# Optimization experiments

Hardware: AMD Instinct MI355X
Metric: run time of the kernel (lower is better)

## Reference

```python
import math
import jax, jax.numpy as jnp
import numpy as np

N_FLOWS = 5
DIM = 64
NH = 128          # hidden multiplier -> hidden width = DIM*NH = 8192
BATCH = 4096


def _masks(out_f, in_f, dim):
    od, idd = out_f // dim, in_f // dim
    mask_d = np.zeros((out_f, in_f), np.float32)
    mask_o = np.ones((out_f, in_f), np.float32)
    for i in range(dim):
        mask_d[i * od:(i + 1) * od, i * idd:(i + 1) * idd] = 1.0
        mask_o[i * od:(i + 1) * od, i * idd:] = 0.0
    return jnp.asarray(mask_d), jnp.asarray(mask_o)

MASK_D1, MASK_O1 = _masks(DIM * NH, DIM, DIM)   # layer 1: (H, D)
MASK_D2, MASK_O2 = _masks(DIM, DIM * NH, DIM)   # layer 2: (D, H)


def masked_weight(x, W, dw, b, mask_d, mask_o, dim, grad=None):
    """MaskedWeight.forward. W:(out,in), dw:(out,1), b:(out,)."""
    out_f, in_f = W.shape
    od, idd = out_f // dim, in_f // dim
    w = jnp.exp(W) * mask_d + W * mask_o                 # (out, in)
    wsn = jnp.sum(w * w, axis=-1, keepdims=True)         # (out, 1)
    wn = jnp.exp(dw) * w / jnp.sqrt(wsn)                 # weight-normalized
    wpl = dw + W - 0.5 * jnp.log(wsn)                    # (out, in)
    # extract diagonal blocks of wpl^T: (dim, idd, od)
    blocks = wpl.reshape(dim, od, dim, idd)
    wpl_t = blocks[np.arange(dim), :, np.arange(dim), :].transpose(0, 2, 1)
    y = x @ wn.T + b                                     # (B, out)
    g = wpl_t.transpose(0, 2, 1)                         # (dim, od, idd)
    if grad is None:
        new_grad = jnp.broadcast_to(g[None], (x.shape[0],) + g.shape)
    else:
        # logsumexp over contracted block axis: out (B, dim, od, b_prev)
        new_grad = jax.nn.logsumexp(
            g[None, :, :, None, :] + jnp.swapaxes(grad, -2, -1)[:, :, None, :, :],
            axis=-1)
    return y, new_grad


def tanh_layer(x, grad):
    g = -2.0 * (x - math.log(2.0) + jax.nn.softplus(-2.0 * x))
    return jnp.tanh(x), g.reshape(grad.shape) + grad


def bnaf_flow(x, W1, d1, b1, W2, d2, b2, gate):
    h, g = masked_weight(x, W1, d1, b1, MASK_D1, MASK_O1, DIM)
    h, g = tanh_layer(h, g)
    y, g = masked_weight(h, W2, d2, b2, MASK_D2, MASK_O2, DIM, grad=g)
    grad = g[:, :, 0, 0]                                  # (B, DIM) -- squeeze
    if gate is None:                                      # res=None (last flow)
        return y, jnp.sum(grad, axis=-1)
    s = jax.nn.sigmoid(gate)                              # res='gated'
    out = s * y + (1.0 - s) * x
    ld = jnp.sum(jax.nn.softplus(grad + gate) - jax.nn.softplus(gate), axis=-1)
    return out, ld


def setup_inputs() -> dict:
    key = jax.random.key(0)
    ks = jax.random.split(key, 8)
    H = DIM * NH
    return {
        "x":  jax.random.normal(ks[0], (BATCH, DIM), jnp.float32),
        "W1": jax.random.normal(ks[1], (N_FLOWS, H, DIM), jnp.float32) * 0.1,
        "d1": jax.random.normal(ks[2], (N_FLOWS, H, 1), jnp.float32) * 0.1,
        "b1": jax.random.normal(ks[3], (N_FLOWS, H), jnp.float32) * 0.01,
        "W2": jax.random.normal(ks[4], (N_FLOWS, DIM, H), jnp.float32) * 0.1,
        "d2": jax.random.normal(ks[5], (N_FLOWS, DIM, 1), jnp.float32) * 0.1,
        "b2": jax.random.normal(ks[6], (N_FLOWS, DIM), jnp.float32) * 0.01,
        "gates": jax.random.normal(ks[7], (N_FLOWS - 1,), jnp.float32),
    }


def reference(x, W1, d1, b1, W2, d2, b2, gates):
    log_det = jnp.zeros(x.shape[0], x.dtype)
    for f in range(N_FLOWS):
        gate = gates[f] if f < N_FLOWS - 1 else None
        x, ld = bnaf_flow(x, W1[f], d1[f], b1[f], W2[f], d2[f], b2[f], gate)
        log_det = log_det + ld
        if f < N_FLOWS - 1:                               # Permutation 'flip'
            x = x[:, ::-1]
    return x, log_det
```

## Files before the change

kernel.cpp:

```cpp
#include <hip/hip_runtime.h>
#include <hip/hip_bf16.h>
#include <math.h>

#define NFLOWS 5
#define DIMF 64
#define HID 8192
#define BATCHN 4096

typedef unsigned int u32;
typedef __bf16 bf16x8 __attribute__((ext_vector_type(8)));
typedef float f32x4 __attribute__((ext_vector_type(4)));

__device__ __forceinline__ short f2bf_s(float x){
  u32 b = __float_as_uint(x);
  b += 0x7fff + ((b >> 16) & 1);
  return (short)(b >> 16);
}
__device__ __forceinline__ u32 pk_bf16(float a, float b){
#if __has_builtin(__builtin_amdgcn_cvt_pk_bf16_f32)
  typedef __bf16 bf16x2_t __attribute__((ext_vector_type(2)));
  bf16x2_t r = __builtin_amdgcn_cvt_pk_bf16_f32(a, b);
  return __builtin_bit_cast(u32, r);
#else
  u32 x = __float_as_uint(a); x += 0x7fff + ((x >> 16) & 1);
  u32 y = __float_as_uint(b); y += 0x7fff + ((y >> 16) & 1);
  return (x >> 16) | (y & 0xffff0000u);
#endif
}
__device__ __forceinline__ float softplus_f(float z){
  return fmaxf(z, 0.f) + log1pf(__expf(-fabsf(z)));
}

__global__ __launch_bounds__(256) void prep_fused_kernel(
    const float* __restrict__ W1, const float* __restrict__ d1,
    const float* __restrict__ b1,
    const float* __restrict__ W2, const float* __restrict__ d2,
    short* __restrict__ wn1s, short* __restrict__ wn2s,
    float* __restrict__ bec, float* __restrict__ cmax)
{
  __shared__ float g1s[128];
  __shared__ float cbuf[128];
  __shared__ float red[4];
  __shared__ float Msh;

  const int tid  = threadIdx.x;
  const int w    = tid >> 6;
  const int lane = tid & 63;
  const int f    = blockIdx.x >> 6;
  const int i    = blockIdx.x & 63;

  {
    const int ks2 = lane >> 5, q = (lane & 31) >> 3, j = lane & 7;
    #pragma unroll 4
    for (int it = 0; it < 32; ++it) {
      int rr = w * 32 + it;
      size_t R = (size_t)(f * HID + i * 128 + rr);
      float Wv = W1[R * 64 + lane];
      float wv = (lane == i) ? __expf(Wv) : ((lane < i) ? Wv : 0.f);
      float sq = wv * wv;
      #pragma unroll
      for (int m = 1; m < 64; m <<= 1) sq += __shfl_xor(sq, m, 64);
      float d1v = d1[R];
      float sc = __expf(d1v) * rsqrtf(sq);
      int nt = rr >> 4, n16 = rr & 15;
      size_t dst = ((((size_t)(f * 64 + i) * 8 + nt) * 2 + ks2) << 9)
                 + ((q * 16 + n16) << 3) + j;
      wn1s[dst] = f2bf_s(wv * sc);
      if (lane == i) g1s[rr] = d1v + Wv - 0.5f * __logf(sq);
    }
  }
  __syncthreads();

  const float* Wrow = W2 + ((size_t)(f * DIMF + i)) * HID;
  const float d2v = d2[f * DIMF + i];

  float part = 0.f;
  #pragma unroll
  for (int it = 0; it < 4; ++it) {
    int k0 = it * 2048 + tid * 8;
    int kb = k0 >> 7;
    float4 a = *(const float4*)(Wrow + k0);
    float4 b = *(const float4*)(Wrow + k0 + 4);
    float wv[8] = {a.x, a.y, a.z, a.w, b.x, b.y, b.z, b.w};
    if (kb == i) {
      #pragma unroll
      for (int e = 0; e < 8; ++e) wv[e] = __expf(wv[e]);
    } else if (kb > i) {
      #pragma unroll
      for (int e = 0; e < 8; ++e) wv[e] = 0.f;
    }
    #pragma unroll
    for (int e = 0; e < 8; ++e) part = fmaf(wv[e], wv[e], part);
  }
  #pragma unroll
  for (int m = 1; m < 64; m <<= 1) part += __shfl_xor(part, m, 64);
  if (lane == 0) red[w] = part;
  __syncthreads();
  float wsn = red[0] + red[1] + red[2] + red[3];
  float ls = __logf(wsn);
  float sc = __expf(d2v) * rsqrtf(wsn);

  const int mt2 = i >> 4, c16r = i & 15;
  #pragma unroll
  for (int it = 0; it < 4; ++it) {
    int k0 = it * 2048 + tid * 8;
    int kb = k0 >> 7;
    float4 a = *(const float4*)(Wrow + k0);
    float4 b = *(const float4*)(Wrow + k0 + 4);
    float wv[8] = {a.x, a.y, a.z, a.w, b.x, b.y, b.z, b.w};
    if (kb == i) {
      int rr0 = k0 - i * 128;
      #pragma unroll
      for (int e = 0; e < 8; ++e) {
        cbuf[rr0 + e] = g1s[rr0 + e] + d2v + wv[e] - 0.5f * ls;
        wv[e] = __expf(wv[e]);
      }
    } else if (kb > i) {
      #pragma unroll
      for (int e = 0; e < 8; ++e) wv[e] = 0.f;
    }
    int ib = k0 >> 7, ks = (k0 >> 5) & 3, qq = (k0 >> 3) & 3;
    size_t dst = ((((size_t)(f * 64 + ib) * 4 + ks) * 4 + mt2) << 9)
               + ((qq * 16 + c16r) << 3);
    uint4 pk4;
    pk4.x = pk_bf16(wv[0]*sc, wv[1]*sc); pk4.y = pk_bf16(wv[2]*sc, wv[3]*sc);
    pk4.z = pk_bf16(wv[4]*sc, wv[5]*sc); pk4.w = pk_bf16(wv[6]*sc, wv[7]*sc);
    *(uint4*)(wn2s + dst) = pk4;
  }
  __syncthreads();

  if (w == 0) {
    float m = fmaxf(cbuf[lane], cbuf[lane + 64]);
    #pragma unroll
    for (int s = 1; s < 64; s <<= 1) m = fmaxf(m, __shfl_xor(m, s, 64));
    if (lane == 0) { cmax[f * DIMF + i] = m; Msh = m; }
  }
  __syncthreads();
  float M = Msh;

  if (tid < 128) {
    int k = i * 128 + tid;
    float2 v;
    v.x = b1[f * HID + k];
    v.y = 4.f * __expf(cbuf[tid] - M);
    *(float2*)(bec + (((size_t)(f * HID + k)) << 1)) = v;
  }
}

__global__ __launch_bounds__(1024, 4)
void bnaf_main_kernel(
    const float* __restrict__ x_in,
    const float* __restrict__ b2,
    const float* __restrict__ gates,
    const short* __restrict__ wn1s,
    const short* __restrict__ wn2s,
    const float* __restrict__ bec, const float* __restrict__ cmax,
    float* __restrict__ out)
{
  __shared__ __attribute__((aligned(16))) char smem[146816];
  float* xs  = (float*)smem;
  short* xbS = (short*)(smem + 4352);
  float* ldp = (float*)(smem + 145792);

  const int tid  = threadIdx.x;
  const int w    = tid >> 6;
  const int lane = tid & 63;
  const int c16  = lane & 15;
  const int q    = lane >> 4;
  const int r0   = blockIdx.x * 16;

  short* tbuf0 = (short*)(smem + 6528 + w * 8704);
  short* tbuf1 = (short*)(smem + 6528 + w * 8704 + 4352);

  {
    int row = tid >> 6, col = tid & 63;
    float v = x_in[((size_t)(r0 + row) << 6) | col];
    xs[row * 68 + col] = v;
    xbS[(col >> 3) * 136 + row * 8 + (col & 7)] = f2bf_s(v);
  }
  float ldtot = 0.f;
  __syncthreads();

  #pragma unroll 1
  for (int f = 0; f < NFLOWS; ++f) {
    const float gatev = (f < NFLOWS - 1) ? gates[f] : 0.f;
    const float spg   = (f < NFLOWS - 1) ? softplus_f(gatev) : 0.f;

    f32x4 yacc[4];
    #pragma unroll
    for (int n = 0; n < 4; ++n) yacc[n] = f32x4{0.f, 0.f, 0.f, 0.f};
    float ldacc = 0.f;

    #pragma unroll 1
    for (int ii = 0; ii < 4; ++ii) {
      const int i = ii * 16 + w;
      short* tb = (ii & 1) ? tbuf1 : tbuf0;
      const short* p1l = wn1s + (((size_t)(f * 64 + i)) << 13) + lane * 8;
      const float* becp = bec + (((size_t)(f * HID + i * 128 + q * 4)) << 1);
      const bool hiHalf = (i >= 32);

      float s0 = 0.f, s1 = 0.f;
      f32x4 dd[4];

      {
        const bf16x8 xa0 = *(const bf16x8*)(xbS + q * 136 + c16 * 8);
        #pragma unroll
        for (int nt = 0; nt < 4; ++nt) {
          f32x4 z = {0.f, 0.f, 0.f, 0.f};
          bf16x8 bw0 = *(const bf16x8*)(p1l + nt * 1024);
          dd[nt] = __builtin_amdgcn_mfma_f32_16x16x32_bf16(bw0, xa0, z, 0, 0, 0);
        }
        if (hiHalf) {
          const bf16x8 xa1 = *(const bf16x8*)(xbS + (4 + q) * 136 + c16 * 8);
          #pragma unroll
          for (int nt = 0; nt < 4; ++nt) {
            bf16x8 bw1 = *(const bf16x8*)(p1l + nt * 1024 + 512);
            dd[nt] = __builtin_amdgcn_mfma_f32_16x16x32_bf16(bw1, xa1, dd[nt], 0, 0, 0);
          }
        }
      }
      #pragma unroll
      for (int nt = 0; nt < 4; ++nt) {
        float4 e0 = *(const float4*)(becp + nt * 32);
        float4 e1 = *(const float4*)(becp + nt * 32 + 4);
        float t[4];
        #pragma unroll
        for (int r = 0; r < 4; ++r) {
          float bb = (r == 0) ? e0.x : (r == 1) ? e0.z : (r == 2) ? e1.x : e1.z;
          float ee = (r == 0) ? e0.y : (r == 1) ? e0.w : (r == 2) ? e1.y : e1.w;
          float h  = dd[nt][r] + bb;
          float up = __expf(-2.f * fabsf(h));
          float vp = __builtin_amdgcn_rcpf(1.f + up);
          float ta = fmaf(-2.f * up, vp, 1.f);
          t[r] = copysignf(ta, h);
          float c1 = ee * up, c2 = vp * vp;
          if (r & 1) s1 = fmaf(c1, c2, s1); else s0 = fmaf(c1, c2, s0);
        }
        uint2 pk; pk.x = pk_bf16(t[0], t[1]); pk.y = pk_bf16(t[2], t[3]);
        *(uint2*)(tb + c16 * 136 + nt * 16 + q * 4) = pk;
      }

      if (ii > 0) {
        const int ip = i - 16;
        short* tp = ((ii - 1) & 1) ? tbuf1 : tbuf0;
        asm volatile("s_waitcnt lgkmcnt(0)" ::: "memory");
        const short* p2l = wn2s + (((size_t)(f * 64 + ip)) << 13) + lane * 8;
        const int mt0 = ip >> 4;
        #pragma unroll
        for (int ks = 0; ks < 4; ++ks) {
          bf16x8 tfrag = *(const bf16x8*)(tp + c16 * 136 + ks * 32 + q * 8);
          #pragma unroll
          for (int mt = 0; mt < 4; ++mt) {
            if (mt >= mt0) {
              bf16x8 wb = *(const bf16x8*)(p2l + (ks * 4 + mt) * 512);
              yacc[mt] = __builtin_amdgcn_mfma_f32_16x16x32_bf16(wb, tfrag, yacc[mt], 0, 0, 0);
            }
          }
        }
      }

      {
        const bf16x8 xa0 = *(const bf16x8*)(xbS + q * 136 + c16 * 8);
        #pragma unroll
        for (int nt = 0; nt < 4; ++nt) {
          f32x4 z = {0.f, 0.f, 0.f, 0.f};
          bf16x8 bw0 = *(const bf16x8*)(p1l + (nt + 4) * 1024);
          dd[nt] = __builtin_amdgcn_mfma_f32_16x16x32_bf16(bw0, xa0, z, 0, 0, 0);
        }
        if (hiHalf) {
          const bf16x8 xa1 = *(const bf16x8*)(xbS + (4 + q) * 136 + c16 * 8);
          #pragma unroll
          for (int nt = 0; nt < 4; ++nt) {
            bf16x8 bw1 = *(const bf16x8*)(p1l + (nt + 4) * 1024 + 512);
            dd[nt] = __builtin_amdgcn_mfma_f32_16x16x32_bf16(bw1, xa1, dd[nt], 0, 0, 0);
          }
        }
      }
      #pragma unroll
      for (int nt = 0; nt < 4; ++nt) {
        float4 e0 = *(const float4*)(becp + (nt + 4) * 32);
        float4 e1 = *(const float4*)(becp + (nt + 4) * 32 + 4);
        float t[4];
        #pragma unroll
        for (int r = 0; r < 4; ++r) {
          float bb = (r == 0) ? e0.x : (r == 1) ? e0.z : (r == 2) ? e1.x : e1.z;
          float ee = (r == 0) ? e0.y : (r == 1) ? e0.w : (r == 2) ? e1.y : e1.w;
          float h  = dd[nt][r] + bb;
          float up = __expf(-2.f * fabsf(h));
          float vp = __builtin_amdgcn_rcpf(1.f + up);
          float ta = fmaf(-2.f * up, vp, 1.f);
          t[r] = copysignf(ta, h);
          float c1 = ee * up, c2 = vp * vp;
          if (r & 1) s1 = fmaf(c1, c2, s1); else s0 = fmaf(c1, c2, s0);
        }
        uint2 pk; pk.x = pk_bf16(t[0], t[1]); pk.y = pk_bf16(t[2], t[3]);
        *(uint2*)(tb + c16 * 136 + (nt + 4) * 16 + q * 4) = pk;
      }

      float sacc = s0 + s1;
      sacc += __shfl_xor(sacc, 16, 64);
      sacc += __shfl_xor(sacc, 32, 64);
      const float Mi = cmax[f * DIMF + i];
      float grad = Mi + __logf(sacc);
      ldacc += (f < NFLOWS - 1) ? (softplus_f(grad + gatev) - spg) : grad;
    }

    {
      const int ip = 48 + w;
      asm volatile("s_waitcnt lgkmcnt(0)" ::: "memory");
      const short* p2l = wn2s + (((size_t)(f * 64 + ip)) << 13) + lane * 8;
      const int mt0 = ip >> 4;
      #pragma unroll
      for (int ks = 0; ks < 4; ++ks) {
        bf16x8 tfrag = *(const bf16x8*)(tbuf1 + c16 * 136 + ks * 32 + q * 8);
        #pragma unroll
        for (int mt = 0; mt < 4; ++mt) {
          if (mt >= mt0) {
            bf16x8 wb = *(const bf16x8*)(p2l + (ks * 4 + mt) * 512);
            yacc[mt] = __builtin_amdgcn_mfma_f32_16x16x32_bf16(wb, tfrag, yacc[mt], 0, 0, 0);
          }
        }
      }
    }

    float* ypw = (float*)(smem + 6528 + w * 8704);
    #pragma unroll
    for (int mt = 0; mt < 4; ++mt)
      #pragma unroll
      for (int r = 0; r < 4; ++r)
        ypw[(mt * 4 + r) * 65 + lane] = yacc[mt][r];
    if (q == 0) ldp[w * 16 + c16] = ldacc;
    __syncthreads();

    float sgate = 0.f;
    if (f < NFLOWS - 1) sgate = __builtin_amdgcn_rcpf(1.f + __expf(-gatev));
    int row = tid >> 6, col = tid & 63;
    int idx = ((col >> 4) * 4 + (col & 3)) * 65 + (((col >> 2) & 3) * 16 + row);
    float v = b2[f * DIMF + col];
    #pragma unroll
    for (int ww = 0; ww < 16; ++ww)
      v += ((const float*)(smem + 6528 + ww * 8704))[idx];
    float nx = 0.f; int nrow = 0, ncol = 0;
    if (f < NFLOWS - 1) {
      float xv = xs[row * 68 + col];
      nx = fmaf(sgate, v - xv, xv);
      nrow = row; ncol = 63 - col;
    } else {
      out[((size_t)(r0 + row) << 6) | col] = v;
    }
    if (tid < 16) {
      float a = 0.f;
      #pragma unroll
      for (int ww = 0; ww < 16; ++ww) a += ldp[ww * 16 + tid];
      ldtot += a;
    }
    __syncthreads();
    if (f < NFLOWS - 1) {
      xs[nrow * 68 + ncol] = nx;
      xbS[(ncol >> 3) * 136 + nrow * 8 + (ncol & 7)] = f2bf_s(nx);
      __syncthreads();
    }
  }

  if (tid < 16) out[(size_t)BATCHN * DIMF + r0 + tid] = ldtot;
}

extern "C" void kernel_launch(void* const* d_in, const int* in_sizes, int n_in,
                              void* d_out, int out_size, void* d_ws, size_t ws_size,
                              hipStream_t stream)
{
  const float* x     = (const float*)d_in[0];
  const float* W1    = (const float*)d_in[1];
  const float* d1    = (const float*)d_in[2];
  const float* b1    = (const float*)d_in[3];
  const float* W2    = (const float*)d_in[4];
  const float* d2    = (const float*)d_in[5];
  const float* b2    = (const float*)d_in[6];
  const float* gates = (const float*)d_in[7];
  float* out = (float*)d_out;

  char* ws = (char*)d_ws;
  short* wn1s  = (short*)ws;
  short* wn2s  = (short*)(ws + 5242880);
  float* bec   = (float*)(ws + 10485760);
  float* cmaxp = (float*)(ws + 10813440);

  hipLaunchKernelGGL(prep_fused_kernel, dim3(320), dim3(256), 0, stream,
                     W1, d1, b1, W2, d2, wn1s, wn2s, bec, cmaxp);
  hipLaunchKernelGGL(bnaf_main_kernel, dim3(256), dim3(1024), 0, stream,
                     x, b2, gates, wn1s, wn2s, bec, cmaxp, out);
}
```

Measured before the change: 322.3 us.

## Halve main-kernel block rows, widen prep kernel, fold bias into MFMA accumulator

The main kernel now processes 8 batch rows per block with 8 waves (512 blocks), padding the MFMA input to 16 rows with zeros and halving LDS use so more blocks can be resident. Each wave now loops over 8 hidden blocks instead of 4, and the waves hand off in steps of 8. The layer-1 bias is loaded directly as the MFMA accumulator initialiser, and the interleaved bias/exp buffer is replaced by a plain exp-constant array. The prep kernel uses 1024 threads so each thread reads its W2 slice once instead of twice. The trade-off is that half of each MFMA's rows are wasted padding, and every block re-reads the full weight set, doubling total weight traffic.

```diff
diff --git a/kernel.cpp b/kernel.cpp
--- a/kernel.cpp
+++ b/kernel.cpp
@@ -31,16 +31,15 @@
   return fmaxf(z, 0.f) + log1pf(__expf(-fabsf(z)));
 }
 
-__global__ __launch_bounds__(256) void prep_fused_kernel(
+__global__ __launch_bounds__(1024) void prep_fused_kernel(
     const float* __restrict__ W1, const float* __restrict__ d1,
-    const float* __restrict__ b1,
     const float* __restrict__ W2, const float* __restrict__ d2,
     short* __restrict__ wn1s, short* __restrict__ wn2s,
-    float* __restrict__ bec, float* __restrict__ cmax)
+    float* __restrict__ expc4, float* __restrict__ cmax)
 {
   __shared__ float g1s[128];
   __shared__ float cbuf[128];
-  __shared__ float red[4];
+  __shared__ float red[16];
   __shared__ float Msh;
 
   const int tid  = threadIdx.x;
@@ -51,9 +50,9 @@
 
   {
     const int ks2 = lane >> 5, q = (lane & 31) >> 3, j = lane & 7;
-    #pragma unroll 4
-    for (int it = 0; it < 32; ++it) {
-      int rr = w * 32 + it;
+    #pragma unroll
+    for (int it = 0; it < 8; ++it) {
+      int rr = w * 8 + it;
       size_t R = (size_t)(f * HID + i * 128 + rr);
       float Wv = W1[R * 64 + lane];
       float wv = (lane == i) ? __expf(Wv) : ((lane < i) ? Wv : 0.f);
@@ -73,58 +72,46 @@
 
   const float* Wrow = W2 + ((size_t)(f * DIMF + i)) * HID;
   const float d2v = d2[f * DIMF + i];
-
+  const int k0 = tid * 8;
+  const int kb = tid >> 4;
+  float4 a = *(const float4*)(Wrow + k0);
+  float4 b = *(const float4*)(Wrow + k0 + 4);
+  float wv[8] = {a.x, a.y, a.z, a.w, b.x, b.y, b.z, b.w};
+  const bool diag = (kb == i);
+  float cv[8];
+  float mv[8];
+  #pragma unroll
+  for (int e = 0; e < 8; ++e) {
+    if (diag)        { cv[e] = g1s[(k0 - i * 128) + e] + d2v + wv[e]; mv[e] = __expf(wv[e]); }
+    else if (kb > i) { mv[e] = 0.f; }
+    else             { mv[e] = wv[e]; }
+  }
   float part = 0.f;
   #pragma unroll
-  for (int it = 0; it < 4; ++it) {
-    int k0 = it * 2048 + tid * 8;
-    int kb = k0 >> 7;
-    float4 a = *(const float4*)(Wrow + k0);
-    float4 b = *(const float4*)(Wrow + k0 + 4);
-    float wv[8] = {a.x, a.y, a.z, a.w, b.x, b.y, b.z, b.w};
-    if (kb == i) {
-      #pragma unroll
-      for (int e = 0; e < 8; ++e) wv[e] = __expf(wv[e]);
-    } else if (kb > i) {
-      #pragma unroll
-      for (int e = 0; e < 8; ++e) wv[e] = 0.f;
-    }
-    #pragma unroll
-    for (int e = 0; e < 8; ++e) part = fmaf(wv[e], wv[e], part);
-  }
+  for (int e = 0; e < 8; ++e) part = fmaf(mv[e], mv[e], part);
   #pragma unroll
   for (int m = 1; m < 64; m <<= 1) part += __shfl_xor(part, m, 64);
   if (lane == 0) red[w] = part;
   __syncthreads();
-  float wsn = red[0] + red[1] + red[2] + red[3];
+  float wsn = 0.f;
+  #pragma unroll
+  for (int e = 0; e < 16; ++e) wsn += red[e];
   float ls = __logf(wsn);
-  float sc = __expf(d2v) * rsqrtf(wsn);
-
-  const int mt2 = i >> 4, c16r = i & 15;
-  #pragma unroll
-  for (int it = 0; it < 4; ++it) {
-    int k0 = it * 2048 + tid * 8;
-    int kb = k0 >> 7;
-    float4 a = *(const float4*)(Wrow + k0);
-    float4 b = *(const float4*)(Wrow + k0 + 4);
-    float wv[8] = {a.x, a.y, a.z, a.w, b.x, b.y, b.z, b.w};
-    if (kb == i) {
-      int rr0 = k0 - i * 128;
-      #pragma unroll
-      for (int e = 0; e < 8; ++e) {
-        cbuf[rr0 + e] = g1s[rr0 + e] + d2v + wv[e] - 0.5f * ls;
-        wv[e] = __expf(wv[e]);
-      }
-    } else if (kb > i) {
-      #pragma unroll
-      for (int e = 0; e < 8; ++e) wv[e] = 0.f;
-    }
-    int ib = k0 >> 7, ks = (k0 >> 5) & 3, qq = (k0 >> 3) & 3;
-    size_t dst = ((((size_t)(f * 64 + ib) * 4 + ks) * 4 + mt2) << 9)
+  float sc2 = __expf(d2v) * rsqrtf(wsn);
+
+  if (diag) {
+    int rr0 = k0 - i * 128;
+    #pragma unroll
+    for (int e = 0; e < 8; ++e) cbuf[rr0 + e] = cv[e] - 0.5f * ls;
+  }
+  {
+    int ks = (k0 >> 5) & 3, qq = (k0 >> 3) & 3;
+    int mt2 = i >> 4, c16r = i & 15;
+    size_t dst = ((((size_t)(f * 64 + kb) * 4 + ks) * 4 + mt2) << 9)
                + ((qq * 16 + c16r) << 3);
     uint4 pk4;
-    pk4.x = pk_bf16(wv[0]*sc, wv[1]*sc); pk4.y = pk_bf16(wv[2]*sc, wv[3]*sc);
-    pk4.z = pk_bf16(wv[4]*sc, wv[5]*sc); pk4.w = pk_bf16(wv[6]*sc, wv[7]*sc);
+    pk4.x = pk_bf16(mv[0]*sc2, mv[1]*sc2); pk4.y = pk_bf16(mv[2]*sc2, mv[3]*sc2);
+    pk4.z = pk_bf16(mv[4]*sc2, mv[5]*sc2); pk4.w = pk_bf16(mv[6]*sc2, mv[7]*sc2);
     *(uint4*)(wn2s + dst) = pk4;
   }
   __syncthreads();
@@ -136,47 +123,40 @@
     if (lane == 0) { cmax[f * DIMF + i] = m; Msh = m; }
   }
   __syncthreads();
-  float M = Msh;
-
-  if (tid < 128) {
-    int k = i * 128 + tid;
-    float2 v;
-    v.x = b1[f * HID + k];
-    v.y = 4.f * __expf(cbuf[tid] - M);
-    *(float2*)(bec + (((size_t)(f * HID + k)) << 1)) = v;
-  }
-}
-
-__global__ __launch_bounds__(1024, 4)
+  if (tid < 128) expc4[f * HID + i * 128 + tid] = 4.f * __expf(cbuf[tid] - Msh);
+}
+
+__global__ __launch_bounds__(512, 4)
 void bnaf_main_kernel(
     const float* __restrict__ x_in,
-    const float* __restrict__ b2,
+    const float* __restrict__ b1, const float* __restrict__ b2,
     const float* __restrict__ gates,
     const short* __restrict__ wn1s,
     const short* __restrict__ wn2s,
-    const float* __restrict__ bec, const float* __restrict__ cmax,
+    const float* __restrict__ expc4, const float* __restrict__ cmax,
     float* __restrict__ out)
 {
-  __shared__ __attribute__((aligned(16))) char smem[146816];
+  __shared__ __attribute__((aligned(16))) char smem[74496];
   float* xs  = (float*)smem;
-  short* xbS = (short*)(smem + 4352);
-  float* ldp = (float*)(smem + 145792);
+  short* xbS = (short*)(smem + 2176);
+  float* ldp = (float*)(smem + 73984);
 
   const int tid  = threadIdx.x;
   const int w    = tid >> 6;
   const int lane = tid & 63;
   const int c16  = lane & 15;
   const int q    = lane >> 4;
-  const int r0   = blockIdx.x * 16;
-
-  short* tbuf0 = (short*)(smem + 6528 + w * 8704);
-  short* tbuf1 = (short*)(smem + 6528 + w * 8704 + 4352);
+  const int r0   = blockIdx.x * 8;
+
+  short* tbuf0 = (short*)(smem + 4352 + w * 8704);
+  short* tbuf1 = (short*)(smem + 4352 + w * 8704 + 4352);
 
   {
     int row = tid >> 6, col = tid & 63;
     float v = x_in[((size_t)(r0 + row) << 6) | col];
     xs[row * 68 + col] = v;
     xbS[(col >> 3) * 136 + row * 8 + (col & 7)] = f2bf_s(v);
+    xbS[(col >> 3) * 136 + (row + 8) * 8 + (col & 7)] = 0;
   }
   float ldtot = 0.f;
   __syncthreads();
@@ -186,49 +166,48 @@
     const float gatev = (f < NFLOWS - 1) ? gates[f] : 0.f;
     const float spg   = (f < NFLOWS - 1) ? softplus_f(gatev) : 0.f;
 
+    const bf16x8 xa0 = *(const bf16x8*)(xbS + q * 136 + c16 * 8);
+    const bf16x8 xa1 = *(const bf16x8*)(xbS + (4 + q) * 136 + c16 * 8);
+
     f32x4 yacc[4];
     #pragma unroll
     for (int n = 0; n < 4; ++n) yacc[n] = f32x4{0.f, 0.f, 0.f, 0.f};
     float ldacc = 0.f;
 
     #pragma unroll 1
-    for (int ii = 0; ii < 4; ++ii) {
-      const int i = ii * 16 + w;
+    for (int ii = 0; ii < 8; ++ii) {
+      const int i = ii * 8 + w;
       short* tb = (ii & 1) ? tbuf1 : tbuf0;
       const short* p1l = wn1s + (((size_t)(f * 64 + i)) << 13) + lane * 8;
-      const float* becp = bec + (((size_t)(f * HID + i * 128 + q * 4)) << 1);
+      const float* b1p = b1    + f * HID + i * 128 + q * 4;
+      const float* ecp = expc4 + f * HID + i * 128 + q * 4;
       const bool hiHalf = (i >= 32);
 
       float s0 = 0.f, s1 = 0.f;
       f32x4 dd[4];
 
-      {
-        const bf16x8 xa0 = *(const bf16x8*)(xbS + q * 136 + c16 * 8);
+      #pragma unroll
+      for (int nt = 0; nt < 4; ++nt) {
+        float4 b1q = *(const float4*)(b1p + nt * 16);
+        f32x4 z = {b1q.x, b1q.y, b1q.z, b1q.w};
+        bf16x8 bw0 = *(const bf16x8*)(p1l + nt * 1024);
+        dd[nt] = __builtin_amdgcn_mfma_f32_16x16x32_bf16(bw0, xa0, z, 0, 0, 0);
+      }
+      if (hiHalf) {
         #pragma unroll
         for (int nt = 0; nt < 4; ++nt) {
-          f32x4 z = {0.f, 0.f, 0.f, 0.f};
-          bf16x8 bw0 = *(const bf16x8*)(p1l + nt * 1024);
-          dd[nt] = __builtin_amdgcn_mfma_f32_16x16x32_bf16(bw0, xa0, z, 0, 0, 0);
-        }
-        if (hiHalf) {
-          const bf16x8 xa1 = *(const bf16x8*)(xbS + (4 + q) * 136 + c16 * 8);
-          #pragma unroll
-          for (int nt = 0; nt < 4; ++nt) {
-            bf16x8 bw1 = *(const bf16x8*)(p1l + nt * 1024 + 512);
-            dd[nt] = __builtin_amdgcn_mfma_f32_16x16x32_bf16(bw1, xa1, dd[nt], 0, 0, 0);
-          }
+          bf16x8 bw1 = *(const bf16x8*)(p1l + nt * 1024 + 512);
+          dd[nt] = __builtin_amdgcn_mfma_f32_16x16x32_bf16(bw1, xa1, dd[nt], 0, 0, 0);
         }
       }
       #pragma unroll
       for (int nt = 0; nt < 4; ++nt) {
-        float4 e0 = *(const float4*)(becp + nt * 32);
-        float4 e1 = *(const float4*)(becp + nt * 32 + 4);
+        float4 ecq = *(const float4*)(ecp + nt * 16);
         float t[4];
         #pragma unroll
         for (int r = 0; r < 4; ++r) {
-          float bb = (r == 0) ? e0.x : (r == 1) ? e0.z : (r == 2) ? e1.x : e1.z;
-          float ee = (r == 0) ? e0.y : (r == 1) ? e0.w : (r == 2) ? e1.y : e1.w;
-          float h  = dd[nt][r] + bb;
+          float ee = (r == 0) ? ecq.x : (r == 1) ? ecq.y : (r == 2) ? ecq.z : ecq.w;
+          float h  = dd[nt][r];
           float up = __expf(-2.f * fabsf(h));
           float vp = __builtin_amdgcn_rcpf(1.f + up);
           float ta = fmaf(-2.f * up, vp, 1.f);
@@ -241,7 +220,7 @@
       }
 
       if (ii > 0) {
-        const int ip = i - 16;
+        const int ip = i - 8;
         short* tp = ((ii - 1) & 1) ? tbuf1 : tbuf0;
         asm volatile("s_waitcnt lgkmcnt(0)" ::: "memory");
         const short* p2l = wn2s + (((size_t)(f * 64 + ip)) << 13) + lane * 8;
@@ -259,33 +238,28 @@
         }
       }
 
-      {
-        const bf16x8 xa0 = *(const bf16x8*)(xbS + q * 136 + c16 * 8);
+      #pragma unroll
+      for (int nt = 0; nt < 4; ++nt) {
+        float4 b1q = *(const float4*)(b1p + (nt + 4) * 16);
+        f32x4 z = {b1q.x, b1q.y, b1q.z, b1q.w};
+        bf16x8 bw0 = *(const bf16x8*)(p1l + (nt + 4) * 1024);
+        dd[nt] = __builtin_amdgcn_mfma_f32_16x16x32_bf16(bw0, xa0, z, 0, 0, 0);
+      }
+      if (hiHalf) {
         #pragma unroll
         for (int nt = 0; nt < 4; ++nt) {
-          f32x4 z = {0.f, 0.f, 0.f, 0.f};
-          bf16x8 bw0 = *(const bf16x8*)(p1l + (nt + 4) * 1024);
-          dd[nt] = __builtin_amdgcn_mfma_f32_16x16x32_bf16(bw0, xa0, z, 0, 0, 0);
-        }
-        if (hiHalf) {
-          const bf16x8 xa1 = *(const bf16x8*)(xbS + (4 + q) * 136 + c16 * 8);
-          #pragma unroll
-          for (int nt = 0; nt < 4; ++nt) {
-            bf16x8 bw1 = *(const bf16x8*)(p1l + (nt + 4) * 1024 + 512);
-            dd[nt] = __builtin_amdgcn_mfma_f32_16x16x32_bf16(bw1, xa1, dd[nt], 0, 0, 0);
-          }
+          bf16x8 bw1 = *(const bf16x8*)(p1l + (nt + 4) * 1024 + 512);
+          dd[nt] = __builtin_amdgcn_mfma_f32_16x16x32_bf16(bw1, xa1, dd[nt], 0, 0, 0);
         }
       }
       #pragma unroll
       for (int nt = 0; nt < 4; ++nt) {
-        float4 e0 = *(const float4*)(becp + (nt + 4) * 32);
-        float4 e1 = *(const float4*)(becp + (nt + 4) * 32 + 4);
+        float4 ecq = *(const float4*)(ecp + (nt + 4) * 16);
         float t[4];
         #pragma unroll
         for (int r = 0; r < 4; ++r) {
-          float bb = (r == 0) ? e0.x : (r == 1) ? e0.z : (r == 2) ? e1.x : e1.z;
-          float ee = (r == 0) ? e0.y : (r == 1) ? e0.w : (r == 2) ? e1.y : e1.w;
-          float h  = dd[nt][r] + bb;
+          float ee = (r == 0) ? ecq.x : (r == 1) ? ecq.y : (r == 2) ? ecq.z : ecq.w;
+          float h  = dd[nt][r];
           float up = __expf(-2.f * fabsf(h));
           float vp = __builtin_amdgcn_rcpf(1.f + up);
           float ta = fmaf(-2.f * up, vp, 1.f);
@@ -306,7 +280,7 @@
     }
 
     {
-      const int ip = 48 + w;
+      const int ip = 56 + w;
       asm volatile("s_waitcnt lgkmcnt(0)" ::: "memory");
       const short* p2l = wn2s + (((size_t)(f * 64 + ip)) << 13) + lane * 8;
       const int mt0 = ip >> 4;
@@ -323,7 +297,7 @@
       }
     }
 
-    float* ypw = (float*)(smem + 6528 + w * 8704);
+    float* ypw = (float*)(smem + 4352 + w * 8704);
     #pragma unroll
     for (int mt = 0; mt < 4; ++mt)
       #pragma unroll
@@ -338,31 +312,31 @@
     int idx = ((col >> 4) * 4 + (col & 3)) * 65 + (((col >> 2) & 3) * 16 + row);
     float v = b2[f * DIMF + col];
     #pragma unroll
-    for (int ww = 0; ww < 16; ++ww)
-      v += ((const float*)(smem + 6528 + ww * 8704))[idx];
-    float nx = 0.f; int nrow = 0, ncol = 0;
+    for (int ww = 0; ww < 8; ++ww)
+      v += ((const float*)(smem + 4352 + ww * 8704))[idx];
+    float nx = 0.f; int ncol = 0;
     if (f < NFLOWS - 1) {
       float xv = xs[row * 68 + col];
       nx = fmaf(sgate, v - xv, xv);
-      nrow = row; ncol = 63 - col;
+      ncol = 63 - col;
     } else {
       out[((size_t)(r0 + row) << 6) | col] = v;
     }
-    if (tid < 16) {
+    if (tid < 8) {
       float a = 0.f;
       #pragma unroll
-      for (int ww = 0; ww < 16; ++ww) a += ldp[ww * 16 + tid];
+      for (int ww = 0; ww < 8; ++ww) a += ldp[ww * 16 + tid];
       ldtot += a;
     }
     __syncthreads();
     if (f < NFLOWS - 1) {
-      xs[nrow * 68 + ncol] = nx;
-      xbS[(ncol >> 3) * 136 + nrow * 8 + (ncol & 7)] = f2bf_s(nx);
+      xs[row * 68 + ncol] = nx;
+      xbS[(ncol >> 3) * 136 + row * 8 + (ncol & 7)] = f2bf_s(nx);
       __syncthreads();
     }
   }
 
-  if (tid < 16) out[(size_t)BATCHN * DIMF + r0 + tid] = ldtot;
+  if (tid < 8) out[(size_t)BATCHN * DIMF + r0 + tid] = ldtot;
 }
 
 extern "C" void kernel_launch(void* const* d_in, const int* in_sizes, int n_in,
@@ -382,11 +356,11 @@
   char* ws = (char*)d_ws;
   short* wn1s  = (short*)ws;
   short* wn2s  = (short*)(ws + 5242880);
-  float* bec   = (float*)(ws + 10485760);
-  float* cmaxp = (float*)(ws + 10813440);
-
-  hipLaunchKernelGGL(prep_fused_kernel, dim3(320), dim3(256), 0, stream,
-                     W1, d1, b1, W2, d2, wn1s, wn2s, bec, cmaxp);
-  hipLaunchKernelGGL(bnaf_main_kernel, dim3(256), dim3(1024), 0, stream,
-                     x, b2, gates, wn1s, wn2s, bec, cmaxp, out);
-}
+  float* expc4 = (float*)(ws + 10485760);
+  float* cmaxp = (float*)(ws + 10649600);
+
+  hipLaunchKernelGGL(prep_fused_kernel, dim3(320), dim3(1024), 0, stream,
+                     W1, d1, W2, d2, wn1s, wn2s, expc4, cmaxp);
+  hipLaunchKernelGGL(bnaf_main_kernel, dim3(512), dim3(512), 0, stream,
+                     x, b1, b2, gates, wn1s, wn2s, expc4, cmaxp, out);
+}
```

After: 406.8 us. +26.2%, slower.
